# Kernel tuning notes

Hardware: AMD Instinct MI355X
Metric: run time of the kernel (lower is better)

Reference implementation:

```python
import jax, jax.numpy as jnp
import numpy as np

N_EMBD = 1024
N_HEAD = 16


def setup_inputs() -> dict:
    key = jax.random.key(0)
    k1, k2, k3 = jax.random.split(key, 3)
    x = jax.random.normal(k1, (4, 2048, N_EMBD), dtype=jnp.float32)
    w_attn = jax.random.normal(k2, (N_EMBD, 3 * N_EMBD), dtype=jnp.float32) * (N_EMBD ** -0.5)
    w_proj = jax.random.normal(k3, (N_EMBD, N_EMBD), dtype=jnp.float32) * (N_EMBD ** -0.5)
    return {"x": x, "w_attn": w_attn, "w_proj": w_proj}


def reference(x, w_attn, w_proj):
    B, T, C = x.shape
    H = N_HEAD
    D = C // H  # head dim
    qkv = x @ w_attn  # [B,T,3C]
    q, k, v = jnp.split(qkv, 3, axis=-1)
    # [B,T,C] -> [B,H,T,D]
    q = q.reshape(B, T, H, D).transpose(0, 2, 1, 3)
    k = k.reshape(B, T, H, D).transpose(0, 2, 1, 3)
    v = v.reshape(B, T, H, D).transpose(0, 2, 1, 3)
    scale = 1.0 / jnp.sqrt(jnp.asarray(D, dtype=x.dtype))
    att = jnp.einsum('bhqd,bhkd->bhqk', q, k) * scale  # [B,H,T,T]
    causal = jnp.tril(jnp.ones((T, T), dtype=bool))
    att = jnp.where(causal, att, jnp.asarray(-jnp.inf, dtype=att.dtype))
    att = jax.nn.softmax(att, axis=-1)
    y = jnp.einsum('bhqk,bhkd->bhqd', att, v)  # [B,H,T,D]
    y = y.transpose(0, 2, 1, 3).reshape(B, T, C)
    return y @ w_proj
```

## Files before the change

### kernel.cpp

```cpp
#include <hip/hip_runtime.h>
#include <math.h>


typedef unsigned short ushort_t;
typedef __attribute__((ext_vector_type(8))) short bf16x8;
typedef __attribute__((ext_vector_type(4))) float f32x4;

#define MFMA16(a, b, c) __builtin_amdgcn_mfma_f32_16x16x32_bf16((a), (b), (c), 0, 0, 0)

#define CP_ASYNC16(lds, gp)                                                        \
    __builtin_amdgcn_global_load_lds(                                              \
        (const __attribute__((address_space(1))) void*)(gp),                       \
        (__attribute__((address_space(3))) void*)(lds), 16, 0, 0)

#define SCALE2 0.1803368801111204f

__device__ __forceinline__ ushort_t bf16r(float x) {
    unsigned int u = __float_as_uint(x);
    u += 0x7FFFu + ((u >> 16) & 1u);
    return (ushort_t)(u >> 16);
}

__device__ __forceinline__ unsigned cvt_pk_bf16(float lo, float hi) {
    unsigned r;
    asm("v_cvt_pk_bf16_f32 %0, %1, %2" : "=v"(r) : "v"(lo), "v"(hi));
    return r;
}
__device__ __forceinline__ void pl32_swap(unsigned& a, unsigned& c) {
    asm("v_permlane32_swap_b32 %0, %1" : "+v"(a), "+v"(c));
}
__device__ __forceinline__ void pl16_swap(unsigned& a, unsigned& c) {
    asm("v_permlane16_swap_b32 %0, %1" : "+v"(a), "+v"(c));
}


__global__ __launch_bounds__(256) void cast_f32_bf16(const float4* __restrict__ src,
                                                     ushort4* __restrict__ dst) {
    int i = blockIdx.x * 256 + threadIdx.x;
    float4 v = src[i];
    ushort4 o;
    o.x = bf16r(v.x); o.y = bf16r(v.y); o.z = bf16r(v.z); o.w = bf16r(v.w);
    dst[i] = o;
}

__global__ __launch_bounds__(256) void transpose_cast(const float* __restrict__ src,
                                                      ushort_t* __restrict__ dst,
                                                      int R, int Cc) {
    __shared__ float tile[32][33];
    const int tx = threadIdx.x, ty = threadIdx.y;
    const int c0 = blockIdx.x * 32, r0 = blockIdx.y * 32;
#pragma unroll
    for (int i = 0; i < 4; ++i)
        tile[ty + i * 8][tx] = src[(size_t)(r0 + ty + i * 8) * Cc + c0 + tx];
    __syncthreads();
#pragma unroll
    for (int i = 0; i < 4; ++i)
        dst[(size_t)(c0 + ty + i * 8) * R + r0 + tx] = bf16r(tile[tx][ty + i * 8]);
}

__global__ __launch_bounds__(256)
void gemm_bf16(const ushort_t* __restrict__ A, const ushort_t* __restrict__ Bt,
               int K, int mode,
               ushort_t* __restrict__ Qh, ushort_t* __restrict__ Kh,
               ushort_t* __restrict__ Vt, float* __restrict__ Cout) {
    __shared__ ushort_t As[2][128 * 32];
    __shared__ ushort_t Bs[2][128 * 32];
    const int tid = threadIdx.x;
    const int l = tid & 63, w = tid >> 6;
    const int lm = l & 15, lq = l >> 4;
    const int wm = w >> 1, wn = w & 1;
    const int row0 = blockIdx.y * 128, col0 = blockIdx.x * 128;
    const f32x4 zero4 = {0.f, 0.f, 0.f, 0.f};
    const int lqs8 = (lq ^ ((lm >> 1) & 3)) * 8;

    f32x4 acc[4][4];
#pragma unroll
    for (int i = 0; i < 4; ++i)
#pragma unroll
        for (int j = 0; j < 4; ++j) acc[i][j] = zero4;

    const int srow = tid >> 2, slot = tid & 3;
    const int soff = (slot ^ ((srow >> 1) & 3)) * 8;
    const ushort_t* ga0 = A + (size_t)(row0 + srow) * K + soff;
    const ushort_t* ga1 = ga0 + (size_t)64 * K;
    const ushort_t* gb0 = Bt + (size_t)(col0 + srow) * K + soff;
    const ushort_t* gb1 = gb0 + (size_t)64 * K;

    const int aoffb = (wm * 64 + lm) * 32 + lqs8;
    const int boffb = (wn * 64 + lm) * 32 + lqs8;

    auto prefetch = [&](int k0, int dbuf) {
        CP_ASYNC16(&As[dbuf][tid * 8], ga0 + k0);
        CP_ASYNC16(&As[dbuf][(tid + 256) * 8], ga1 + k0);
        CP_ASYNC16(&Bs[dbuf][tid * 8], gb0 + k0);
        CP_ASYNC16(&Bs[dbuf][(tid + 256) * 8], gb1 + k0);
    };

    prefetch(0, 0);
    const int niter = K >> 5;
    for (int it = 0; it < niter; ++it) {
        const int buf = it & 1;
        __syncthreads();
        if (it + 1 < niter) prefetch((it + 1) << 5, buf ^ 1);

        bf16x8 af[4], bfr[4];
#pragma unroll
        for (int i = 0; i < 4; ++i)
            af[i] = *(const bf16x8*)(As[buf] + aoffb + i * (16 * 32));
#pragma unroll
        for (int j = 0; j < 4; ++j)
            bfr[j] = *(const bf16x8*)(Bs[buf] + boffb + j * (16 * 32));
#pragma unroll
        for (int i = 0; i < 4; ++i)
#pragma unroll
            for (int j = 0; j < 4; ++j)
                acc[i][j] = MFMA16(af[i], bfr[j], acc[i][j]);
    }

#pragma unroll
    for (int i = 0; i < 4; ++i) {
#pragma unroll
        for (int j = 0; j < 4; ++j) {
#pragma unroll
            for (int reg = 0; reg < 4; ++reg) {
                const int rr = row0 + wm * 64 + i * 16 + lq * 4 + reg;
                const int cc = col0 + wn * 64 + j * 16 + lm;
                const float v = acc[i][j][reg];
                if (mode == 1) {
                    Cout[(size_t)rr * 1024 + cc] = v;
                } else {
                    const int b = rr >> 11, t = rr & 2047;
                    if (cc < 1024) {
                        const int h = cc >> 6, d = cc & 63;
                        Qh[((size_t)(b * 16 + h) * 2048 + t) * 64 + d] =
                            bf16r(v * SCALE2);
                    } else if (cc < 2048) {
                        const int c2 = cc - 1024, h = c2 >> 6, d = c2 & 63;
                        Kh[((size_t)(b * 16 + h) * 2048 + t) * 64 + d] = bf16r(v);
                    } else {
                        const int c2 = cc - 2048, h = c2 >> 6, d = c2 & 63;
                        Vt[((size_t)(b * 16 + h) * 64 + d) * 2048 + t] = bf16r(v);
                    }
                }
            }
        }
    }
}

__global__ __launch_bounds__(256, 4)
void attn_mfma(const ushort_t* __restrict__ Qh, const ushort_t* __restrict__ Kh,
               const ushort_t* __restrict__ Vt, ushort_t* __restrict__ Y) {
    __shared__ ushort_t Ks[2][4096];
    __shared__ ushort_t Vs[2][4096];
    const int tid = threadIdx.x, l = tid & 63, w = tid >> 6;
    const int lm = l & 15, lq = l >> 4;
    const int bh = blockIdx.x;
    const int pr = blockIdx.y;
    const int qbA = pr, qbB = 31 - pr;
    const int b = bh >> 4, h = bh & 15;
    const f32x4 zero4 = {0.f, 0.f, 0.f, 0.f};
    const short oneb = (short)0x3F80;
    const bf16x8 onesf = {oneb, oneb, oneb, oneb, oneb, oneb, oneb, oneb};
    const int lqs8 = (lq ^ ((lm >> 1) & 3)) * 8;

    bf16x8 qf[2][2];
    {
        const ushort_t* qA = Qh + ((size_t)bh * 2048 + qbA * 64 + w * 16 + lm) * 64 + lq * 8;
        const ushort_t* qB = Qh + ((size_t)bh * 2048 + qbB * 64 + w * 16 + lm) * 64 + lq * 8;
        qf[0][0] = *(const bf16x8*)(qA);
        qf[0][1] = *(const bf16x8*)(qA + 32);
        qf[1][0] = *(const bf16x8*)(qB);
        qf[1][1] = *(const bf16x8*)(qB + 32);
    }

    f32x4 O[2][4], Ol[2];
#pragma unroll
    for (int q = 0; q < 2; ++q) {
        Ol[q] = zero4;
#pragma unroll
        for (int i = 0; i < 4; ++i) O[q][i] = zero4;
    }

    const int srow = tid >> 2, slot = tid & 3;
    const int srcoff = ((slot ^ ((srow >> 1) & 3)) * 8);
    const ushort_t* gKr = Kh + ((size_t)bh * 2048 + srow) * 64 + srcoff;
    const ushort_t* gVr = Vt + ((size_t)bh * 64 + srow) * 2048 + srcoff;

    auto prefetch = [&](int jbn, int dbuf) {
        const ushort_t* gk = gKr + (size_t)jbn * 4096;
        const ushort_t* gv = gVr + jbn * 64;
        CP_ASYNC16(&Ks[dbuf][tid * 8], gk);
        CP_ASYNC16(&Ks[dbuf][2048 + tid * 8], gk + 32);
        CP_ASYNC16(&Vs[dbuf][tid * 8], gv);
        CP_ASYNC16(&Vs[dbuf][2048 + tid * 8], gv + 32);
    };

    auto process = [&](const bf16x8 (&kf)[4][2], const ushort_t* Vb,
                       const bf16x8 (&qfr)[2], f32x4 (&Or)[4], f32x4& Olr,
                       bool diag) {
        f32x4 st[4];
        __builtin_amdgcn_s_setprio(1);
#pragma unroll
        for (int n = 0; n < 4; ++n) {
            f32x4 s_acc = zero4;
            s_acc = MFMA16(kf[n][0], qfr[0], s_acc);
            s_acc = MFMA16(kf[n][1], qfr[1], s_acc);
            st[n] = s_acc;
        }
        __builtin_amdgcn_s_setprio(0);

        float p[4][4];
#pragma unroll
        for (int n = 0; n < 4; ++n)
#pragma unroll
            for (int reg = 0; reg < 4; ++reg)
                p[n][reg] = __builtin_amdgcn_exp2f(st[n][reg]);
        if (diag) {
            const int qloc = w * 16 + lm;
#pragma unroll
            for (int n = 0; n < 4; ++n)
#pragma unroll
                for (int reg = 0; reg < 4; ++reg)
                    if (n * 16 + lq * 4 + reg > qloc) p[n][reg] = 0.f;
        }

        unsigned cpk[4][2];
#pragma unroll
        for (int n = 0; n < 4; ++n) {
            cpk[n][0] = cvt_pk_bf16(p[n][0], p[n][1]);
            cpk[n][1] = cvt_pk_bf16(p[n][2], p[n][3]);
        }

        union U8 { unsigned u[4]; bf16x8 v; };
        bf16x8 pf0, pf1;
        {
            unsigned z00 = cpk[0][0], z10 = cpk[1][0];
            unsigned z01 = cpk[0][1], z11 = cpk[1][1];
            pl32_swap(z00, z10); pl16_swap(z00, z10);
            pl32_swap(z01, z11); pl16_swap(z01, z11);
            U8 t0; t0.u[0] = z00; t0.u[1] = z01; t0.u[2] = z10; t0.u[3] = z11;
            pf0 = t0.v;
            unsigned y00 = cpk[2][0], y10 = cpk[3][0];
            unsigned y01 = cpk[2][1], y11 = cpk[3][1];
            pl32_swap(y00, y10); pl16_swap(y00, y10);
            pl32_swap(y01, y11); pl16_swap(y01, y11);
            U8 t1; t1.u[0] = y00; t1.u[1] = y01; t1.u[2] = y10; t1.u[3] = y11;
            pf1 = t1.v;
        }

        __builtin_amdgcn_s_setprio(1);
#pragma unroll
        for (int dn = 0; dn < 4; ++dn) {
            const bf16x8 vf0 = *(const bf16x8*)(Vb + (dn * 16 + lm) * 32 + lqs8);
            const bf16x8 vf1 = *(const bf16x8*)(Vb + 2048 + (dn * 16 + lm) * 32 + lqs8);
            Or[dn] = MFMA16(pf0, vf0, Or[dn]);
            Or[dn] = MFMA16(pf1, vf1, Or[dn]);
        }
        Olr = MFMA16(pf0, onesf, Olr);
        Olr = MFMA16(pf1, onesf, Olr);
        __builtin_amdgcn_s_setprio(0);
    };

    prefetch(0, 0);
    for (int jb = 0; jb <= qbB; ++jb) {
        const int buf = jb & 1;
        __syncthreads();
        if (jb < qbB) prefetch(jb + 1, buf ^ 1);

        const ushort_t* Kb = Ks[buf];
        const ushort_t* Vb = Vs[buf];
        bf16x8 kf[4][2];
#pragma unroll
        for (int n = 0; n < 4; ++n) {
            kf[n][0] = *(const bf16x8*)(Kb + (n * 16 + lm) * 32 + lqs8);
            kf[n][1] = *(const bf16x8*)(Kb + 2048 + (n * 16 + lm) * 32 + lqs8);
        }

        process(kf, Vb, qf[1], O[1], Ol[1], jb == qbB);
        if (jb <= qbA)
            process(kf, Vb, qf[0], O[0], Ol[0], jb == qbA);
    }

#pragma unroll
    for (int qs = 0; qs < 2; ++qs) {
        const int tq = (qs ? qbB : qbA) * 64;
#pragma unroll
        for (int reg = 0; reg < 4; ++reg) {
            const float inv = 1.f / Ol[qs][reg];
            const size_t row = (size_t)b * 2048 + tq + w * 16 + lq * 4 + reg;
#pragma unroll
            for (int dn = 0; dn < 4; ++dn)
                Y[row * 1024 + h * 64 + dn * 16 + lm] = bf16r(O[qs][dn][reg] * inv);
        }
    }
}


extern "C" void kernel_launch(void* const* d_in, const int* in_sizes, int n_in,
                              void* d_out, int out_size, void* d_ws, size_t ws_size,
                              hipStream_t stream) {
    const float* x      = (const float*)d_in[0];
    const float* w_attn = (const float*)d_in[1];
    const float* w_proj = (const float*)d_in[2];
    float* out = (float*)d_out;

    char* ws = (char*)d_ws;
    ushort_t* xb   = (ushort_t*)(ws);
    ushort_t* watT = (ushort_t*)(ws + 16777216);
    ushort_t* wpjT = (ushort_t*)(ws + 23068672);
    ushort_t* Qh   = (ushort_t*)(ws + 25165824);
    ushort_t* Kh   = (ushort_t*)(ws + 41943040);
    ushort_t* Vt   = (ushort_t*)(ws + 58720256);
    ushort_t* Y    = (ushort_t*)(ws + 75497472);

    hipLaunchKernelGGL(cast_f32_bf16, dim3(8192), dim3(256), 0, stream,
                       (const float4*)x, (ushort4*)xb);
    hipLaunchKernelGGL(transpose_cast, dim3(96, 32), dim3(32, 8), 0, stream,
                       w_attn, watT, 1024, 3072);
    hipLaunchKernelGGL(transpose_cast, dim3(32, 32), dim3(32, 8), 0, stream,
                       w_proj, wpjT, 1024, 1024);

    hipLaunchKernelGGL(gemm_bf16, dim3(24, 64), dim3(256), 0, stream,
                       xb, watT, 1024, 0, Qh, Kh, Vt, (float*)nullptr);

    hipLaunchKernelGGL(attn_mfma, dim3(64, 16), dim3(256), 0, stream,
                       Qh, Kh, Vt, Y);

    hipLaunchKernelGGL(gemm_bf16, dim3(8, 64), dim3(256), 0, stream,
                       Y, wpjT, 1024, 1, (ushort_t*)nullptr, (ushort_t*)nullptr,
                       (ushort_t*)nullptr, out);
}
```

Baseline: 261.7 us.

## Replace 128x128 GEMM with 256x256 tiled, finely pipelined 8-wave GEMM

Both projection GEMMs move from a 128x128 tile with 4 waves and K-step 32 to a 256x256 tile with 8 waves and K-step 64. The main loop interleaves quarter-tile LDS reads, async global-to-LDS staging and MFMA blocks under explicit barriers, vmcnt waits and setprio. Block IDs are remapped across 8 groups to improve L2 locality. The aim is more data reuse per loaded byte and better overlap of memory traffic with MFMA work. The cost is heavy register pressure from 128 accumulator floats per thread, and fewer blocks for the small output-projection GEMM (128 blocks).

```diff
diff --git a/kernel.cpp b/kernel.cpp
--- a/kernel.cpp
+++ b/kernel.cpp
@@ -14,6 +14,18 @@
         (__attribute__((address_space(3))) void*)(lds), 16, 0, 0)
 
 #define SCALE2 0.1803368801111204f
+
+#define BAR() __builtin_amdgcn_s_barrier()
+#define WAITBAR4()                                           \
+    do {                                                     \
+        asm volatile("s_waitcnt vmcnt(4)" ::: "memory");     \
+        __builtin_amdgcn_s_barrier();                        \
+    } while (0)
+#define WAITBAR0()                                           \
+    do {                                                     \
+        asm volatile("s_waitcnt vmcnt(0)" ::: "memory");     \
+        __builtin_amdgcn_s_barrier();                        \
+    } while (0)
 
 __device__ __forceinline__ ushort_t bf16r(float x) {
     unsigned int u = __float_as_uint(x);
@@ -58,77 +70,163 @@
         dst[(size_t)(c0 + ty + i * 8) * R + r0 + tx] = bf16r(tile[tx][ty + i * 8]);
 }
 
-__global__ __launch_bounds__(256)
-void gemm_bf16(const ushort_t* __restrict__ A, const ushort_t* __restrict__ Bt,
-               int K, int mode,
-               ushort_t* __restrict__ Qh, ushort_t* __restrict__ Kh,
-               ushort_t* __restrict__ Vt, float* __restrict__ Cout) {
-    __shared__ ushort_t As[2][128 * 32];
-    __shared__ ushort_t Bs[2][128 * 32];
+__global__ __launch_bounds__(512, 2)
+void gemm256(const ushort_t* __restrict__ A, const ushort_t* __restrict__ Bt,
+             int K, int mode,
+             ushort_t* __restrict__ Qh, ushort_t* __restrict__ Kh,
+             ushort_t* __restrict__ Vt, float* __restrict__ Cout, int nbx) {
+    __shared__ __align__(16) ushort_t As[2][16384];
+    __shared__ __align__(16) ushort_t Bs[2][16384];
     const int tid = threadIdx.x;
     const int l = tid & 63, w = tid >> 6;
     const int lm = l & 15, lq = l >> 4;
-    const int wm = w >> 1, wn = w & 1;
-    const int row0 = blockIdx.y * 128, col0 = blockIdx.x * 128;
-    const f32x4 zero4 = {0.f, 0.f, 0.f, 0.f};
-    const int lqs8 = (lq ^ ((lm >> 1) & 3)) * 8;
-
-    f32x4 acc[4][4];
-#pragma unroll
-    for (int i = 0; i < 4; ++i)
-#pragma unroll
-        for (int j = 0; j < 4; ++j) acc[i][j] = zero4;
-
-    const int srow = tid >> 2, slot = tid & 3;
-    const int soff = (slot ^ ((srow >> 1) & 3)) * 8;
-    const ushort_t* ga0 = A + (size_t)(row0 + srow) * K + soff;
-    const ushort_t* ga1 = ga0 + (size_t)64 * K;
-    const ushort_t* gb0 = Bt + (size_t)(col0 + srow) * K + soff;
-    const ushort_t* gb1 = gb0 + (size_t)64 * K;
-
-    const int aoffb = (wm * 64 + lm) * 32 + lqs8;
-    const int boffb = (wn * 64 + lm) * 32 + lqs8;
-
-    auto prefetch = [&](int k0, int dbuf) {
-        CP_ASYNC16(&As[dbuf][tid * 8], ga0 + k0);
-        CP_ASYNC16(&As[dbuf][(tid + 256) * 8], ga1 + k0);
-        CP_ASYNC16(&Bs[dbuf][tid * 8], gb0 + k0);
-        CP_ASYNC16(&Bs[dbuf][(tid + 256) * 8], gb1 + k0);
-    };
-
-    prefetch(0, 0);
-    const int niter = K >> 5;
+    const int wm = w >> 2, wn = w & 3;
+
+    int bid = blockIdx.x;
+    const int cpx = gridDim.x >> 3;
+    bid = (bid & 7) * cpx + (bid >> 3);
+    const int by = bid / nbx, bx = bid - by * nbx;
+    const int row0 = by * 256, col0 = bx * 256;
+
+    const int srow = tid >> 3, sslot = tid & 7;
+    const int ssw = (sslot ^ (srow & 7)) * 8;
+    const ushort_t* gA = A + (size_t)(row0 + srow) * K + ssw;
+    const ushort_t* gB = Bt + (size_t)(col0 + srow) * K + ssw;
+
+    auto stageA = [&](int dbuf, int hm, int T) {
+        const ushort_t* s = gA + (size_t)(hm * 128) * K + T * 64;
+        CP_ASYNC16(&As[dbuf][hm * 8192 + tid * 8], s);
+        CP_ASYNC16(&As[dbuf][hm * 8192 + 4096 + tid * 8], s + (size_t)64 * K);
+    };
+    auto stageB = [&](int dbuf, int hm, int T) {
+        const ushort_t* s = gB + (size_t)(hm * 128) * K + T * 64;
+        CP_ASYNC16(&Bs[dbuf][hm * 8192 + tid * 8], s);
+        CP_ASYNC16(&Bs[dbuf][hm * 8192 + 4096 + tid * 8], s + (size_t)64 * K);
+    };
+
+    const int arow0 = wm * 128 + lm;
+    const int brow0 = wn * 64 + lm;
+    const int lsw = lm & 7;
+
+    f32x4 acc[8][4];
+#pragma unroll
+    for (int i = 0; i < 8; ++i)
+#pragma unroll
+        for (int j = 0; j < 4; ++j) acc[i][j] = (f32x4){0.f, 0.f, 0.f, 0.f};
+
+    bf16x8 af[4][2];
+    bf16x8 bq[2][2][2];
+
+    auto ldA = [&](int d, int qm) {
+#pragma unroll
+        for (int mf = 0; mf < 4; ++mf) {
+            const int r = arow0 + qm * 64 + mf * 16;
+#pragma unroll
+            for (int ks = 0; ks < 2; ++ks)
+                af[mf][ks] =
+                    *(const bf16x8*)(&As[d][r * 64 + (((ks << 2) | lq) ^ lsw) * 8]);
+        }
+    };
+    auto ldB = [&](int d, int qn) {
+#pragma unroll
+        for (int nf = 0; nf < 2; ++nf) {
+            const int r = brow0 + qn * 32 + nf * 16;
+#pragma unroll
+            for (int ks = 0; ks < 2; ++ks)
+                bq[qn][nf][ks] =
+                    *(const bf16x8*)(&Bs[d][r * 64 + (((ks << 2) | lq) ^ lsw) * 8]);
+        }
+    };
+    auto mma = [&](int qm, int qn) {
+        __builtin_amdgcn_s_setprio(1);
+#pragma unroll
+        for (int mf = 0; mf < 4; ++mf)
+#pragma unroll
+            for (int nf = 0; nf < 2; ++nf) {
+                f32x4 c = acc[qm * 4 + mf][qn * 2 + nf];
+                c = MFMA16(af[mf][0], bq[qn][nf][0], c);
+                c = MFMA16(af[mf][1], bq[qn][nf][1], c);
+                acc[qm * 4 + mf][qn * 2 + nf] = c;
+            }
+        __builtin_amdgcn_s_setprio(0);
+    };
+
+    stageA(0, 0, 0); stageA(0, 1, 0);
+    stageB(0, 0, 0); stageB(0, 1, 0);
+    stageB(1, 0, 1); stageB(1, 1, 1);
+
+    const int ntiles = K >> 6;
+    const int niter = ntiles >> 1;
+
     for (int it = 0; it < niter; ++it) {
-        const int buf = it & 1;
-        __syncthreads();
-        if (it + 1 < niter) prefetch((it + 1) << 5, buf ^ 1);
-
-        bf16x8 af[4], bfr[4];
-#pragma unroll
-        for (int i = 0; i < 4; ++i)
-            af[i] = *(const bf16x8*)(As[buf] + aoffb + i * (16 * 32));
-#pragma unroll
-        for (int j = 0; j < 4; ++j)
-            bfr[j] = *(const bf16x8*)(Bs[buf] + boffb + j * (16 * 32));
-#pragma unroll
-        for (int i = 0; i < 4; ++i)
-#pragma unroll
-            for (int j = 0; j < 4; ++j)
-                acc[i][j] = MFMA16(af[i], bfr[j], acc[i][j]);
-    }
-
-#pragma unroll
-    for (int i = 0; i < 4; ++i) {
-#pragma unroll
-        for (int j = 0; j < 4; ++j) {
-#pragma unroll
-            for (int reg = 0; reg < 4; ++reg) {
-                const int rr = row0 + wm * 64 + i * 16 + lq * 4 + reg;
-                const int cc = col0 + wn * 64 + j * 16 + lm;
-                const float v = acc[i][j][reg];
-                if (mode == 1) {
-                    Cout[(size_t)rr * 1024 + cc] = v;
-                } else {
+        const int tE = 2 * it, tO = tE + 1;
+        const bool s2 = (tE + 2) < ntiles;
+        const bool s3 = (tE + 3) < ntiles;
+
+        WAITBAR4();
+        ldA(0, 0); ldB(0, 0);
+        stageA(1, 0, tO);
+        BAR();
+        mma(0, 0);
+        BAR();
+        ldB(0, 1);
+        stageA(1, 1, tO);
+        BAR();
+        mma(0, 1);
+        BAR();
+        ldA(0, 1);
+        if (s2) stageB(0, 0, tE + 2);
+        BAR();
+        mma(1, 0);
+        BAR();
+        if (s2) stageB(0, 1, tE + 2);
+        BAR();
+        mma(1, 1);
+        BAR();
+
+        if (it + 1 < niter) { WAITBAR4(); } else { WAITBAR0(); }
+        ldA(1, 0); ldB(1, 0);
+        if (s2) stageA(0, 0, tE + 2);
+        BAR();
+        mma(0, 0);
+        BAR();
+        ldB(1, 1);
+        if (s2) stageA(0, 1, tE + 2);
+        BAR();
+        mma(0, 1);
+        BAR();
+        ldA(1, 1);
+        if (s3) stageB(1, 0, tE + 3);
+        BAR();
+        mma(1, 0);
+        BAR();
+        if (s3) stageB(1, 1, tE + 3);
+        BAR();
+        mma(1, 1);
+        BAR();
+    }
+
+    if (mode == 1) {
+#pragma unroll
+        for (int im = 0; im < 8; ++im)
+#pragma unroll
+            for (int in = 0; in < 4; ++in)
+#pragma unroll
+                for (int reg = 0; reg < 4; ++reg) {
+                    const int rr = row0 + wm * 128 + im * 16 + lq * 4 + reg;
+                    const int cc = col0 + wn * 64 + in * 16 + lm;
+                    Cout[(size_t)rr * 1024 + cc] = acc[im][in][reg];
+                }
+    } else {
+#pragma unroll
+        for (int im = 0; im < 8; ++im) {
+#pragma unroll
+            for (int in = 0; in < 4; ++in) {
+#pragma unroll
+                for (int reg = 0; reg < 4; ++reg) {
+                    const int rr = row0 + wm * 128 + im * 16 + lq * 4 + reg;
+                    const int cc = col0 + wn * 64 + in * 16 + lm;
+                    const float v = acc[im][in][reg];
                     const int b = rr >> 11, t = rr & 2047;
                     if (cc < 1024) {
                         const int h = cc >> 6, d = cc & 63;
@@ -320,13 +418,13 @@
     hipLaunchKernelGGL(transpose_cast, dim3(32, 32), dim3(32, 8), 0, stream,
                        w_proj, wpjT, 1024, 1024);
 
-    hipLaunchKernelGGL(gemm_bf16, dim3(24, 64), dim3(256), 0, stream,
-                       xb, watT, 1024, 0, Qh, Kh, Vt, (float*)nullptr);
+    hipLaunchKernelGGL(gemm256, dim3(384), dim3(512), 0, stream,
+                       xb, watT, 1024, 0, Qh, Kh, Vt, (float*)nullptr, 12);
 
     hipLaunchKernelGGL(attn_mfma, dim3(64, 16), dim3(256), 0, stream,
                        Qh, Kh, Vt, Y);
 
-    hipLaunchKernelGGL(gemm_bf16, dim3(8, 64), dim3(256), 0, stream,
+    hipLaunchKernelGGL(gemm256, dim3(128), dim3(512), 0, stream,
                        Y, wpjT, 1024, 1, (ushort_t*)nullptr, (ushort_t*)nullptr,
-                       (ushort_t*)nullptr, out);
-}
+                       (ushort_t*)nullptr, out, 4);
+}
```

Result: no change. 263.3 us (+0.6%).
